# Kernel tuning notes

Hardware: AMD Instinct MI355X
Metric: run time of the kernel (lower is better)

The kernel has to match this reference:

```python
import jax, jax.numpy as jnp
import numpy as np

B, E, XD = 2, 196608, 128     # batch, num edges (fine nodes), per-edge node feature dim
EIN, EOUT = 4, 128            # edge embedder dims
NREC = 12288                  # receiver (coarse) node count = 12*32^2
LIN, LOUT = EOUT + XD, 256    # output FFN dims


def setup_inputs() -> dict:
    key = jax.random.key(0)
    ks = jax.random.split(key, 8)
    w = lambda k, sh: jax.random.normal(k, sh, jnp.float32) * 0.05
    return {
        "x": jax.random.normal(ks[0], (B, E, XD), jnp.float32),
        "edge_attr": jax.random.normal(ks[1], (E, EIN), jnp.float32),
        "edge_index": jax.random.randint(ks[2], (2, E), 0, NREC, jnp.int32),
        # edge_embedder MLP: Linear(EIN,EOUT) -> SiLU -> Linear(EOUT,EOUT)
        "W1": w(ks[3], (EIN, EOUT)), "b1": jnp.zeros((EOUT,), jnp.float32),
        "W2": w(ks[4], (EOUT, EOUT)), "b2": jnp.zeros((EOUT,), jnp.float32),
        # output FeedForward: Linear(LIN,LOUT) -> SiLU -> Linear(LOUT,LOUT)
        "L1": w(ks[5], (LIN, LOUT)), "c1": jnp.zeros((LOUT,), jnp.float32),
        "L2": w(ks[6], (LOUT, LOUT)), "c2": jnp.zeros((LOUT,), jnp.float32),
    }


def reference(x, edge_attr, edge_index, W1, b1, W2, b2, L1, c1, L2, c2):
    # Edge MLP embed: [E, EIN] -> [E, EOUT]
    h = jax.nn.silu(edge_attr @ W1 + b1) @ W2 + b2
    # Broadcast edge features over batch and concat with per-edge node features
    ef = jnp.broadcast_to(h[None], (x.shape[0], h.shape[0], h.shape[1]))
    v = jnp.concatenate([ef, x], axis=-1)                 # [B, E, EOUT+XD]
    recv = edge_index[1]                                  # [E] in [0, NREC)
    # scatter_sum over edges -> receiver nodes, per batch
    agg = jax.vmap(lambda vb: jax.ops.segment_sum(vb, recv, num_segments=NREC))(v)  # [B, NREC, LIN]
    # Output FFN
    return jax.nn.silu(agg @ L1 + c1) @ L2 + c2           # [B, NREC, LOUT]
```

## Files before the change

kernel.cpp:

```cpp
#include <hip/hip_runtime.h>
#include <hip/hip_bf16.h>
#include <cstdint>
#include <cstddef>

#define B_     2
#define E_     196608
#define XD_    128
#define NREC_  12288
#define EOUT_  128
#define LIN_   256
#define LOUT_  256
#define M_     (B_ * NREC_)

typedef __attribute__((ext_vector_type(8))) short short8;
typedef __attribute__((ext_vector_type(4))) float f32x4;

__device__ __forceinline__ unsigned short f2bf(float f) {
    union { float f; unsigned u; } v; v.f = f;
    unsigned r = v.u + 0x7FFFu + ((v.u >> 16) & 1u);
    return (unsigned short)(r >> 16);
}

__global__ __launch_bounds__(256) void precompute(
        const float* __restrict__ W2, const float* __restrict__ b2,
        const float* __restrict__ L1, const float* __restrict__ L2,
        unsigned short* __restrict__ L1T, unsigned short* __restrict__ L2T,
        float* __restrict__ v) {
    int bid = blockIdx.x;
    int n = threadIdx.x;
    if (bid < 128) {
        int j = bid;
        float a0 = 0.f, a1 = 0.f, a2 = 0.f, a3 = 0.f;
        for (int c = 0; c < 128; c += 4) {
            a0 = fmaf(W2[j * 128 + c + 0], L1[(c + 0) * 256 + n], a0);
            a1 = fmaf(W2[j * 128 + c + 1], L1[(c + 1) * 256 + n], a1);
            a2 = fmaf(W2[j * 128 + c + 2], L1[(c + 2) * 256 + n], a2);
            a3 = fmaf(W2[j * 128 + c + 3], L1[(c + 3) * 256 + n], a3);
        }
        L1T[n * 256 + j] = f2bf((a0 + a1) + (a2 + a3));
        if (j == 0) {
            float s0 = 0.f, s1 = 0.f;
            for (int c = 0; c < 128; c += 2) {
                s0 = fmaf(b2[c + 0], L1[(c + 0) * 256 + n], s0);
                s1 = fmaf(b2[c + 1], L1[(c + 1) * 256 + n], s1);
            }
            v[n] = s0 + s1;
        }
    } else if (bid < 256) {
        int k = bid;
        L1T[n * 256 + k] = f2bf(L1[k * 256 + n]);
    } else {
        int k = bid - 256;
        L2T[n * 256 + k] = f2bf(L2[k * 256 + n]);
    }
}

__global__ __launch_bounds__(256) void count_kernel(const int* __restrict__ recv,
                                                    int* __restrict__ cnt) {
    int e = blockIdx.x * 256 + threadIdx.x;
    if (e < E_) atomicAdd(&cnt[recv[e]], 1);
}

__global__ __launch_bounds__(1024) void scan_kernel(const int* __restrict__ cnt,
                                                    int* __restrict__ rowStart,
                                                    int* __restrict__ cursor) {
    __shared__ int sums[1024];
    int tid = threadIdx.x;
    int base = tid * 12;
    int local[12];
    int s = 0;
    #pragma unroll
    for (int j = 0; j < 12; ++j) { local[j] = s; s += cnt[base + j]; }
    sums[tid] = s;
    __syncthreads();
    for (int off = 1; off < 1024; off <<= 1) {
        int vv = sums[tid];
        int add = (tid >= off) ? sums[tid - off] : 0;
        __syncthreads();
        sums[tid] = vv + add;
        __syncthreads();
    }
    int excl = (tid == 0) ? 0 : sums[tid - 1];
    #pragma unroll
    for (int j = 0; j < 12; ++j) {
        int vv = excl + local[j];
        rowStart[base + j] = vv;
        cursor[base + j] = vv;
    }
    if (tid == 1023) rowStart[NREC_] = excl + s;
}

__global__ __launch_bounds__(256) void fill_kernel(const int* __restrict__ recv,
                                                   int* __restrict__ cursor,
                                                   int* __restrict__ edge_ids) {
    int e = blockIdx.x * 256 + threadIdx.x;
    if (e < E_) {
        int p = atomicAdd(&cursor[recv[e]], 1);
        edge_ids[p] = e;
    }
}

__global__ __launch_bounds__(128) void gather_kernel(
        const float* __restrict__ x, const float* __restrict__ ea,
        const float* __restrict__ W1, const float* __restrict__ b1,
        const int* __restrict__ rowStart, const int* __restrict__ edge_ids,
        unsigned short* __restrict__ agg_bf) {
    int r = blockIdx.x;
    int c = threadIdx.x;
    int k0 = __builtin_amdgcn_readfirstlane(rowStart[r]);
    int k1 = __builtin_amdgcn_readfirstlane(rowStart[r + 1]);
    float w10 = W1[c], w11 = W1[128 + c], w12 = W1[256 + c], w13 = W1[384 + c];
    float bb1 = b1[c];
    const float* xb = x + (size_t)E_ * 128;
    float accS = 0.f, aX0 = 0.f, aX1 = 0.f;
    int k = k0;
    for (; k + 8 <= k1; k += 8) {
        int e[8];
        #pragma unroll
        for (int u = 0; u < 8; ++u)
            e[u] = __builtin_amdgcn_readfirstlane(edge_ids[k + u]);
        float xa[8], xc[8];
        float4 q[8];
        #pragma unroll
        for (int u = 0; u < 8; ++u) {
            xa[u] = x[(size_t)e[u] * 128 + c];
            xc[u] = xb[(size_t)e[u] * 128 + c];
            q[u] = *(const float4*)(ea + (size_t)e[u] * 4);
        }
        #pragma unroll
        for (int u = 0; u < 8; ++u) {
            float p = fmaf(q[u].x, w10, fmaf(q[u].y, w11,
                      fmaf(q[u].z, w12, fmaf(q[u].w, w13, bb1))));
            accS += p / (1.f + __expf(-p));
            aX0 += xa[u];
            aX1 += xc[u];
        }
    }
    for (; k < k1; ++k) {
        int e0 = __builtin_amdgcn_readfirstlane(edge_ids[k]);
        float4 q = *(const float4*)(ea + (size_t)e0 * 4);
        float p = fmaf(q.x, w10, fmaf(q.y, w11, fmaf(q.z, w12, fmaf(q.w, w13, bb1))));
        accS += p / (1.f + __expf(-p));
        aX0 += x[(size_t)e0 * 128 + c];
        aX1 += xb[(size_t)e0 * 128 + c];
    }
    unsigned short sb = f2bf(accS);
    agg_bf[(size_t)r * 256 + c] = sb;
    agg_bf[(size_t)(NREC_ + r) * 256 + c] = sb;
    agg_bf[(size_t)r * 256 + 128 + c] = f2bf(aX0);
    agg_bf[(size_t)(NREC_ + r) * 256 + 128 + c] = f2bf(aX1);
}

__global__ __launch_bounds__(256) void ffn_kernel(
        const unsigned short* __restrict__ agg,
        const unsigned short* __restrict__ L1T, const float* __restrict__ c1,
        const unsigned short* __restrict__ L2T, const float* __restrict__ c2,
        const float* __restrict__ v, const int* __restrict__ cnt,
        float* __restrict__ out) {
    __shared__ unsigned short T[64][264];
    int tid  = threadIdx.x;
    int wave = tid >> 6;
    int lane = tid & 63;
    int quad = lane >> 4;
    int l16  = lane & 15;
    int m0 = blockIdx.x * 64 + wave * 16;

    float cntv[4];
    #pragma unroll
    for (int rr = 0; rr < 4; ++rr) {
        int m = m0 + quad * 4 + rr;
        int r = (m >= NREC_) ? m - NREC_ : m;
        cntv[rr] = (float)cnt[r];
    }

    short8 afrag[8];
    const unsigned short* aptr = agg + (size_t)(m0 + l16) * 256 + quad * 8;
    #pragma unroll
    for (int ks = 0; ks < 8; ++ks)
        afrag[ks] = *(const short8*)(aptr + ks * 32);

    #pragma unroll 2
    for (int nt = 0; nt < 16; ++nt) {
        f32x4 acc = {0.f, 0.f, 0.f, 0.f};
        const unsigned short* bptr = L1T + (size_t)(nt * 16 + l16) * 256 + quad * 8;
        #pragma unroll
        for (int ks = 0; ks < 8; ++ks) {
            short8 bfrag = *(const short8*)(bptr + ks * 32);
            acc = __builtin_amdgcn_mfma_f32_16x16x32_bf16(afrag[ks], bfrag, acc, 0, 0, 0);
        }
        #pragma unroll
        for (int rr = 0; rr < 4; ++rr) {
            int row = quad * 4 + rr;
            int col = nt * 16 + l16;
            float pv = acc[rr] + c1[col] + cntv[rr] * v[col];
            pv = pv / (1.f + __expf(-pv));
            T[wave * 16 + row][col] = f2bf(pv);
        }
    }
    __syncthreads();

    short8 afrag2[8];
    #pragma unroll
    for (int ks = 0; ks < 8; ++ks)
        afrag2[ks] = *(const short8*)&T[wave * 16 + l16][ks * 32 + quad * 8];

    #pragma unroll 2
    for (int nt = 0; nt < 16; ++nt) {
        f32x4 acc = {0.f, 0.f, 0.f, 0.f};
        const unsigned short* bptr = L2T + (size_t)(nt * 16 + l16) * 256 + quad * 8;
        #pragma unroll
        for (int ks = 0; ks < 8; ++ks) {
            short8 bfrag = *(const short8*)(bptr + ks * 32);
            acc = __builtin_amdgcn_mfma_f32_16x16x32_bf16(afrag2[ks], bfrag, acc, 0, 0, 0);
        }
        #pragma unroll
        for (int rr = 0; rr < 4; ++rr) {
            int row = m0 + quad * 4 + rr;
            int col = nt * 16 + l16;
            out[(size_t)row * 256 + col] = acc[rr] + c2[col];
        }
    }
}

extern "C" void kernel_launch(void* const* d_in, const int* in_sizes, int n_in,
                              void* d_out, int out_size, void* d_ws, size_t ws_size,
                              hipStream_t stream) {
    const float* x          = (const float*)d_in[0];
    const float* edge_attr  = (const float*)d_in[1];
    const int*   edge_index = (const int*)d_in[2];
    const float* W1 = (const float*)d_in[3];
    const float* b1 = (const float*)d_in[4];
    const float* W2 = (const float*)d_in[5];
    const float* b2 = (const float*)d_in[6];
    const float* L1 = (const float*)d_in[7];
    const float* c1 = (const float*)d_in[8];
    const float* L2 = (const float*)d_in[9];
    const float* c2 = (const float*)d_in[10];
    float* out = (float*)d_out;

    int* cnt      = (int*)d_ws;
    int* rowStart = cnt + NREC_;
    int* cursor   = rowStart + NREC_ + 4;
    int* edge_ids = cursor + NREC_;
    unsigned short* agg_bf = (unsigned short*)(edge_ids + E_);
    unsigned short* L1T = agg_bf + (size_t)M_ * 256;
    unsigned short* L2T = L1T + 256 * 256;
    float* v = (float*)(L2T + 256 * 256);

    const int* recv = edge_index + E_;

    hipMemsetAsync(cnt, 0, NREC_ * sizeof(int), stream);
    precompute<<<512, 256, 0, stream>>>(W2, b2, L1, L2, L1T, L2T, v);
    count_kernel<<<(E_ + 255) / 256, 256, 0, stream>>>(recv, cnt);
    scan_kernel<<<1, 1024, 0, stream>>>(cnt, rowStart, cursor);
    fill_kernel<<<(E_ + 255) / 256, 256, 0, stream>>>(recv, cursor, edge_ids);
    gather_kernel<<<NREC_, 128, 0, stream>>>(x, edge_attr, W1, b1,
                                             rowStart, edge_ids, agg_bf);
    ffn_kernel<<<M_ / 64, 256, 0, stream>>>(agg_bf, L1T, c1, L2T, c2, v, cnt, out);
}
```

Measured before the change: 414.2 us.

## Fuse count into precompute, vectorize scan/fill/gather, split aggregate buffers

Merges the edge-count atomics into the weight-precompute launch, so one kernel launch goes away. The scan becomes wave-shuffle based, and fill now handles four edges per thread. The gather kernel now splits edges across four slots, with each thread doing float4 loads over four channels, and reduces the partials through shuffles and LDS. This targets latency-bound scalar gathers. The edge-embedding aggregate is stored once rather than duplicated per batch, and the FFN now reads separate S and X buffers using smaller 128-thread blocks. In exchange there is more reduction overhead and a different occupancy profile.

```diff
diff --git a/kernel.cpp b/kernel.cpp
--- a/kernel.cpp
+++ b/kernel.cpp
@@ -21,11 +21,12 @@
     return (unsigned short)(r >> 16);
 }
 
-__global__ __launch_bounds__(256) void precompute(
+__global__ __launch_bounds__(256) void pre_count(
         const float* __restrict__ W2, const float* __restrict__ b2,
         const float* __restrict__ L1, const float* __restrict__ L2,
         unsigned short* __restrict__ L1T, unsigned short* __restrict__ L2T,
-        float* __restrict__ v) {
+        float* __restrict__ v,
+        const int* __restrict__ recv, int* __restrict__ cnt) {
     int bid = blockIdx.x;
     int n = threadIdx.x;
     if (bid < 128) {
@@ -49,135 +50,201 @@
     } else if (bid < 256) {
         int k = bid;
         L1T[n * 256 + k] = f2bf(L1[k * 256 + n]);
-    } else {
+    } else if (bid < 512) {
         int k = bid - 256;
         L2T[n * 256 + k] = f2bf(L2[k * 256 + n]);
-    }
-}
-
-__global__ __launch_bounds__(256) void count_kernel(const int* __restrict__ recv,
-                                                    int* __restrict__ cnt) {
-    int e = blockIdx.x * 256 + threadIdx.x;
-    if (e < E_) atomicAdd(&cnt[recv[e]], 1);
+    } else {
+        int i = (bid - 512) * 1024 + n * 4;
+        int4 rv = *(const int4*)(recv + i);
+        atomicAdd(&cnt[rv.x], 1);
+        atomicAdd(&cnt[rv.y], 1);
+        atomicAdd(&cnt[rv.z], 1);
+        atomicAdd(&cnt[rv.w], 1);
+    }
 }
 
 __global__ __launch_bounds__(1024) void scan_kernel(const int* __restrict__ cnt,
                                                     int* __restrict__ rowStart,
                                                     int* __restrict__ cursor) {
-    __shared__ int sums[1024];
-    int tid = threadIdx.x;
+    __shared__ int wsum[16];
+    int tid  = threadIdx.x;
+    int lane = tid & 63;
+    int wave = tid >> 6;
     int base = tid * 12;
+    int4 c0 = *(const int4*)(cnt + base);
+    int4 c1 = *(const int4*)(cnt + base + 4);
+    int4 c2 = *(const int4*)(cnt + base + 8);
+    int arr[12] = {c0.x, c0.y, c0.z, c0.w, c1.x, c1.y, c1.z, c1.w,
+                   c2.x, c2.y, c2.z, c2.w};
     int local[12];
     int s = 0;
     #pragma unroll
-    for (int j = 0; j < 12; ++j) { local[j] = s; s += cnt[base + j]; }
-    sums[tid] = s;
+    for (int j = 0; j < 12; ++j) { local[j] = s; s += arr[j]; }
+    int inc = s;
+    #pragma unroll
+    for (int off = 1; off < 64; off <<= 1) {
+        int nb = __shfl_up(inc, off, 64);
+        if (lane >= off) inc += nb;
+    }
+    if (lane == 63) wsum[wave] = inc;
     __syncthreads();
-    for (int off = 1; off < 1024; off <<= 1) {
-        int vv = sums[tid];
-        int add = (tid >= off) ? sums[tid - off] : 0;
-        __syncthreads();
-        sums[tid] = vv + add;
-        __syncthreads();
-    }
-    int excl = (tid == 0) ? 0 : sums[tid - 1];
-    #pragma unroll
-    for (int j = 0; j < 12; ++j) {
-        int vv = excl + local[j];
-        rowStart[base + j] = vv;
-        cursor[base + j] = vv;
-    }
-    if (tid == 1023) rowStart[NREC_] = excl + s;
+    if (tid < 64) {
+        int wv = (tid < 16) ? wsum[tid] : 0;
+        #pragma unroll
+        for (int off = 1; off < 16; off <<= 1) {
+            int nb = __shfl_up(wv, off, 64);
+            if (lane >= off) wv += nb;
+        }
+        if (tid < 16) wsum[tid] = wv;
+    }
+    __syncthreads();
+    int wpre = (wave == 0) ? 0 : wsum[wave - 1];
+    int excl = wpre + inc - s;
+    #pragma unroll
+    for (int j = 0; j < 12; ++j) local[j] += excl;
+    *(int4*)(rowStart + base)     = make_int4(local[0], local[1], local[2], local[3]);
+    *(int4*)(rowStart + base + 4) = make_int4(local[4], local[5], local[6], local[7]);
+    *(int4*)(rowStart + base + 8) = make_int4(local[8], local[9], local[10], local[11]);
+    *(int4*)(cursor + base)       = make_int4(local[0], local[1], local[2], local[3]);
+    *(int4*)(cursor + base + 4)   = make_int4(local[4], local[5], local[6], local[7]);
+    *(int4*)(cursor + base + 8)   = make_int4(local[8], local[9], local[10], local[11]);
+    if (tid == 1023) rowStart[NREC_] = wpre + inc;
 }
 
 __global__ __launch_bounds__(256) void fill_kernel(const int* __restrict__ recv,
                                                    int* __restrict__ cursor,
                                                    int* __restrict__ edge_ids) {
-    int e = blockIdx.x * 256 + threadIdx.x;
-    if (e < E_) {
-        int p = atomicAdd(&cursor[recv[e]], 1);
-        edge_ids[p] = e;
-    }
+    int i = (blockIdx.x * 256 + threadIdx.x) * 4;
+    int4 rv = *(const int4*)(recv + i);
+    int p0 = atomicAdd(&cursor[rv.x], 1); edge_ids[p0] = i;
+    int p1 = atomicAdd(&cursor[rv.y], 1); edge_ids[p1] = i + 1;
+    int p2 = atomicAdd(&cursor[rv.z], 1); edge_ids[p2] = i + 2;
+    int p3 = atomicAdd(&cursor[rv.w], 1); edge_ids[p3] = i + 3;
 }
 
 __global__ __launch_bounds__(128) void gather_kernel(
         const float* __restrict__ x, const float* __restrict__ ea,
         const float* __restrict__ W1, const float* __restrict__ b1,
         const int* __restrict__ rowStart, const int* __restrict__ edge_ids,
-        unsigned short* __restrict__ agg_bf) {
-    int r = blockIdx.x;
-    int c = threadIdx.x;
+        unsigned short* __restrict__ aggS, unsigned short* __restrict__ aggX) {
+    __shared__ float red[2][3][128];
+    int r    = blockIdx.x;
+    int t    = threadIdx.x;
+    int wave = t >> 6;
+    int lane = t & 63;
+    int slot = t >> 5;
+    int q4   = (t & 31) * 4;
     int k0 = __builtin_amdgcn_readfirstlane(rowStart[r]);
     int k1 = __builtin_amdgcn_readfirstlane(rowStart[r + 1]);
-    float w10 = W1[c], w11 = W1[128 + c], w12 = W1[256 + c], w13 = W1[384 + c];
-    float bb1 = b1[c];
+    float4 w1r0 = *(const float4*)(W1 + q4);
+    float4 w1r1 = *(const float4*)(W1 + 128 + q4);
+    float4 w1r2 = *(const float4*)(W1 + 256 + q4);
+    float4 w1r3 = *(const float4*)(W1 + 384 + q4);
+    float4 bb   = *(const float4*)(b1 + q4);
     const float* xb = x + (size_t)E_ * 128;
-    float accS = 0.f, aX0 = 0.f, aX1 = 0.f;
-    int k = k0;
-    for (; k + 8 <= k1; k += 8) {
-        int e[8];
-        #pragma unroll
-        for (int u = 0; u < 8; ++u)
-            e[u] = __builtin_amdgcn_readfirstlane(edge_ids[k + u]);
-        float xa[8], xc[8];
-        float4 q[8];
-        #pragma unroll
-        for (int u = 0; u < 8; ++u) {
-            xa[u] = x[(size_t)e[u] * 128 + c];
-            xc[u] = xb[(size_t)e[u] * 128 + c];
-            q[u] = *(const float4*)(ea + (size_t)e[u] * 4);
-        }
-        #pragma unroll
-        for (int u = 0; u < 8; ++u) {
-            float p = fmaf(q[u].x, w10, fmaf(q[u].y, w11,
-                      fmaf(q[u].z, w12, fmaf(q[u].w, w13, bb1))));
-            accS += p / (1.f + __expf(-p));
-            aX0 += xa[u];
-            aX1 += xc[u];
-        }
-    }
-    for (; k < k1; ++k) {
-        int e0 = __builtin_amdgcn_readfirstlane(edge_ids[k]);
-        float4 q = *(const float4*)(ea + (size_t)e0 * 4);
-        float p = fmaf(q.x, w10, fmaf(q.y, w11, fmaf(q.z, w12, fmaf(q.w, w13, bb1))));
-        accS += p / (1.f + __expf(-p));
-        aX0 += x[(size_t)e0 * 128 + c];
-        aX1 += xb[(size_t)e0 * 128 + c];
-    }
-    unsigned short sb = f2bf(accS);
-    agg_bf[(size_t)r * 256 + c] = sb;
-    agg_bf[(size_t)(NREC_ + r) * 256 + c] = sb;
-    agg_bf[(size_t)r * 256 + 128 + c] = f2bf(aX0);
-    agg_bf[(size_t)(NREC_ + r) * 256 + 128 + c] = f2bf(aX1);
-}
-
-__global__ __launch_bounds__(256) void ffn_kernel(
-        const unsigned short* __restrict__ agg,
+    float4 aS = {0.f, 0.f, 0.f, 0.f};
+    float4 a0 = {0.f, 0.f, 0.f, 0.f};
+    float4 a1 = {0.f, 0.f, 0.f, 0.f};
+
+    int k = k0 + slot;
+    for (; k + 4 < k1; k += 8) {
+        int eA = edge_ids[k];
+        int eB = edge_ids[k + 4];
+        float4 xaA = *(const float4*)(x  + (size_t)eA * 128 + q4);
+        float4 xcA = *(const float4*)(xb + (size_t)eA * 128 + q4);
+        float4 qA  = *(const float4*)(ea + (size_t)eA * 4);
+        float4 xaB = *(const float4*)(x  + (size_t)eB * 128 + q4);
+        float4 xcB = *(const float4*)(xb + (size_t)eB * 128 + q4);
+        float4 qB  = *(const float4*)(ea + (size_t)eB * 4);
+        float4 p;
+        p.x = fmaf(qA.x, w1r0.x, fmaf(qA.y, w1r1.x, fmaf(qA.z, w1r2.x, fmaf(qA.w, w1r3.x, bb.x))));
+        p.y = fmaf(qA.x, w1r0.y, fmaf(qA.y, w1r1.y, fmaf(qA.z, w1r2.y, fmaf(qA.w, w1r3.y, bb.y))));
+        p.z = fmaf(qA.x, w1r0.z, fmaf(qA.y, w1r1.z, fmaf(qA.z, w1r2.z, fmaf(qA.w, w1r3.z, bb.z))));
+        p.w = fmaf(qA.x, w1r0.w, fmaf(qA.y, w1r1.w, fmaf(qA.z, w1r2.w, fmaf(qA.w, w1r3.w, bb.w))));
+        aS.x += p.x / (1.f + __expf(-p.x));
+        aS.y += p.y / (1.f + __expf(-p.y));
+        aS.z += p.z / (1.f + __expf(-p.z));
+        aS.w += p.w / (1.f + __expf(-p.w));
+        a0.x += xaA.x; a0.y += xaA.y; a0.z += xaA.z; a0.w += xaA.w;
+        a1.x += xcA.x; a1.y += xcA.y; a1.z += xcA.z; a1.w += xcA.w;
+        p.x = fmaf(qB.x, w1r0.x, fmaf(qB.y, w1r1.x, fmaf(qB.z, w1r2.x, fmaf(qB.w, w1r3.x, bb.x))));
+        p.y = fmaf(qB.x, w1r0.y, fmaf(qB.y, w1r1.y, fmaf(qB.z, w1r2.y, fmaf(qB.w, w1r3.y, bb.y))));
+        p.z = fmaf(qB.x, w1r0.z, fmaf(qB.y, w1r1.z, fmaf(qB.z, w1r2.z, fmaf(qB.w, w1r3.z, bb.z))));
+        p.w = fmaf(qB.x, w1r0.w, fmaf(qB.y, w1r1.w, fmaf(qB.z, w1r2.w, fmaf(qB.w, w1r3.w, bb.w))));
+        aS.x += p.x / (1.f + __expf(-p.x));
+        aS.y += p.y / (1.f + __expf(-p.y));
+        aS.z += p.z / (1.f + __expf(-p.z));
+        aS.w += p.w / (1.f + __expf(-p.w));
+        a0.x += xaB.x; a0.y += xaB.y; a0.z += xaB.z; a0.w += xaB.w;
+        a1.x += xcB.x; a1.y += xcB.y; a1.z += xcB.z; a1.w += xcB.w;
+    }
+    if (k < k1) {
+        int e0 = edge_ids[k];
+        float4 xa = *(const float4*)(x  + (size_t)e0 * 128 + q4);
+        float4 xc = *(const float4*)(xb + (size_t)e0 * 128 + q4);
+        float4 qe = *(const float4*)(ea + (size_t)e0 * 4);
+        float4 p;
+        p.x = fmaf(qe.x, w1r0.x, fmaf(qe.y, w1r1.x, fmaf(qe.z, w1r2.x, fmaf(qe.w, w1r3.x, bb.x))));
+        p.y = fmaf(qe.x, w1r0.y, fmaf(qe.y, w1r1.y, fmaf(qe.z, w1r2.y, fmaf(qe.w, w1r3.y, bb.y))));
+        p.z = fmaf(qe.x, w1r0.z, fmaf(qe.y, w1r1.z, fmaf(qe.z, w1r2.z, fmaf(qe.w, w1r3.z, bb.z))));
+        p.w = fmaf(qe.x, w1r0.w, fmaf(qe.y, w1r1.w, fmaf(qe.z, w1r2.w, fmaf(qe.w, w1r3.w, bb.w))));
+        aS.x += p.x / (1.f + __expf(-p.x));
+        aS.y += p.y / (1.f + __expf(-p.y));
+        aS.z += p.z / (1.f + __expf(-p.z));
+        aS.w += p.w / (1.f + __expf(-p.w));
+        a0.x += xa.x; a0.y += xa.y; a0.z += xa.z; a0.w += xa.w;
+        a1.x += xc.x; a1.y += xc.y; a1.z += xc.z; a1.w += xc.w;
+    }
+    aS.x += __shfl_xor(aS.x, 32, 64); aS.y += __shfl_xor(aS.y, 32, 64);
+    aS.z += __shfl_xor(aS.z, 32, 64); aS.w += __shfl_xor(aS.w, 32, 64);
+    a0.x += __shfl_xor(a0.x, 32, 64); a0.y += __shfl_xor(a0.y, 32, 64);
+    a0.z += __shfl_xor(a0.z, 32, 64); a0.w += __shfl_xor(a0.w, 32, 64);
+    a1.x += __shfl_xor(a1.x, 32, 64); a1.y += __shfl_xor(a1.y, 32, 64);
+    a1.z += __shfl_xor(a1.z, 32, 64); a1.w += __shfl_xor(a1.w, 32, 64);
+    if (lane < 32) {
+        *(float4*)&red[wave][0][q4] = aS;
+        *(float4*)&red[wave][1][q4] = a0;
+        *(float4*)&red[wave][2][q4] = a1;
+    }
+    __syncthreads();
+    float S  = red[0][0][t] + red[1][0][t];
+    float X0 = red[0][1][t] + red[1][1][t];
+    float X1 = red[0][2][t] + red[1][2][t];
+    aggS[(size_t)r * 128 + t] = f2bf(S);
+    aggX[(size_t)r * 128 + t] = f2bf(X0);
+    aggX[(size_t)(NREC_ + r) * 128 + t] = f2bf(X1);
+}
+
+__global__ __launch_bounds__(128) void ffn_kernel(
+        const unsigned short* __restrict__ aggS,
+        const unsigned short* __restrict__ aggX,
         const unsigned short* __restrict__ L1T, const float* __restrict__ c1,
         const unsigned short* __restrict__ L2T, const float* __restrict__ c2,
         const float* __restrict__ v, const int* __restrict__ cnt,
         float* __restrict__ out) {
-    __shared__ unsigned short T[64][264];
+    __shared__ unsigned short T[32][264];
     int tid  = threadIdx.x;
     int wave = tid >> 6;
     int lane = tid & 63;
     int quad = lane >> 4;
     int l16  = lane & 15;
-    int m0 = blockIdx.x * 64 + wave * 16;
+    int m0 = blockIdx.x * 32 + wave * 16;
+    int b  = (blockIdx.x * 32) / NREC_;
+    int r0 = m0 - b * NREC_;
 
     float cntv[4];
     #pragma unroll
-    for (int rr = 0; rr < 4; ++rr) {
-        int m = m0 + quad * 4 + rr;
-        int r = (m >= NREC_) ? m - NREC_ : m;
-        cntv[rr] = (float)cnt[r];
-    }
+    for (int rr = 0; rr < 4; ++rr)
+        cntv[rr] = (float)cnt[r0 + quad * 4 + rr];
 
     short8 afrag[8];
-    const unsigned short* aptr = agg + (size_t)(m0 + l16) * 256 + quad * 8;
-    #pragma unroll
-    for (int ks = 0; ks < 8; ++ks)
-        afrag[ks] = *(const short8*)(aptr + ks * 32);
+    const unsigned short* aS = aggS + (size_t)(r0 + l16) * 128 + quad * 8;
+    const unsigned short* aX = aggX + ((size_t)b * NREC_ + r0 + l16) * 128 + quad * 8;
+    #pragma unroll
+    for (int ks = 0; ks < 4; ++ks) {
+        afrag[ks]     = *(const short8*)(aS + ks * 32);
+        afrag[ks + 4] = *(const short8*)(aX + ks * 32);
+    }
 
     #pragma unroll 2
     for (int nt = 0; nt < 16; ++nt) {
@@ -242,19 +309,19 @@
     int* rowStart = cnt + NREC_;
     int* cursor   = rowStart + NREC_ + 4;
     int* edge_ids = cursor + NREC_;
-    unsigned short* agg_bf = (unsigned short*)(edge_ids + E_);
-    unsigned short* L1T = agg_bf + (size_t)M_ * 256;
+    unsigned short* aggS = (unsigned short*)(edge_ids + E_);
+    unsigned short* aggX = aggS + (size_t)NREC_ * 128;
+    unsigned short* L1T = aggX + (size_t)B_ * NREC_ * 128;
     unsigned short* L2T = L1T + 256 * 256;
     float* v = (float*)(L2T + 256 * 256);
 
     const int* recv = edge_index + E_;
 
     hipMemsetAsync(cnt, 0, NREC_ * sizeof(int), stream);
-    precompute<<<512, 256, 0, stream>>>(W2, b2, L1, L2, L1T, L2T, v);
-    count_kernel<<<(E_ + 255) / 256, 256, 0, stream>>>(recv, cnt);
+    pre_count<<<704, 256, 0, stream>>>(W2, b2, L1, L2, L1T, L2T, v, recv, cnt);
     scan_kernel<<<1, 1024, 0, stream>>>(cnt, rowStart, cursor);
-    fill_kernel<<<(E_ + 255) / 256, 256, 0, stream>>>(recv, cursor, edge_ids);
+    fill_kernel<<<192, 256, 0, stream>>>(recv, cursor, edge_ids);
     gather_kernel<<<NREC_, 128, 0, stream>>>(x, edge_attr, W1, b1,
-                                             rowStart, edge_ids, agg_bf);
-    ffn_kernel<<<M_ / 64, 256, 0, stream>>>(agg_bf, L1T, c1, L2T, c2, v, cnt, out);
-}
+                                             rowStart, edge_ids, aggS, aggX);
+    ffn_kernel<<<M_ / 32, 128, 0, stream>>>(aggS, aggX, L1T, c1, L2T, c2, v, cnt, out);
+}
```

Measured after the change: 396.3 us. 4.3% less time.
